# Optimization experiments

Hardware: AMD Instinct MI355X
Metric: run time of the kernel (lower is better)

The kernel has to match this reference:

```python
import jax, jax.numpy as jnp
import numpy as np

B, S, D, H = 2, 2048, 1024, 16  # batch, seq_len, model dim, heads


def setup_inputs() -> dict:
    key = jax.random.key(0)
    ks = jax.random.split(key, 5)
    return {
        "x": jax.random.normal(ks[0], (B, S, D), jnp.float32),
        "idx": jax.random.randint(ks[1], (B,), 0, S),
        "weight": jnp.float32(0.5),
        "attn_forcing": 1,  # static python flag
        "w_qkv": jax.random.normal(ks[2], (D, 3 * D), jnp.float32) * 0.02,
        "b_qkv": jnp.zeros((3 * D,), jnp.float32),
        "w_proj": jax.random.normal(ks[3], (D, D), jnp.float32) * 0.02,
        "b_proj": jnp.zeros((D,), jnp.float32),
    }


def reference(x, idx, weight, attn_forcing, w_qkv, b_qkv, w_proj, b_proj):
    Bx, Sx, Dm = x.shape
    dh = Dm // H
    # qkv projection (Conv1D: x @ w + b)
    qkv = x @ w_qkv + b_qkv  # [B,S,3D]
    q, k, v = jnp.split(qkv, 3, axis=-1)
    q = q.reshape(Bx, Sx, H, dh).transpose(0, 2, 1, 3)  # [B,H,S,dh]
    k = k.reshape(Bx, Sx, H, dh).transpose(0, 2, 1, 3)
    v = v.reshape(Bx, Sx, H, dh).transpose(0, 2, 1, 3)
    alen = jnp.arange(Sx)
    mask = (alen[None, :] <= alen[:, None]).astype(x.dtype)  # [S,S] causal
    w = jnp.einsum('bhqd,bhkd->bhqk', q, k) / jnp.asarray(np.sqrt(dh), x.dtype)
    w = w * mask + jnp.asarray(-1e9, x.dtype) * (1 - mask)
    w = jax.nn.softmax(w, axis=-1)
    if attn_forcing:
        # post-softmax forcing reweight: positions >= idx scaled by weight, then renorm
        a = jnp.where(alen[None, :] >= idx[:, None], weight, jnp.asarray(1.0, x.dtype))  # [B,S]
        w = w * a[:, None, None, :]
        w = w / jnp.sum(w, axis=-1, keepdims=True)
    out = jnp.einsum('bhqk,bhkd->bhqd', w, v)  # [B,H,S,dh]
    out = out.transpose(0, 2, 1, 3).reshape(Bx, Sx, Dm)  # merge heads
    return out @ w_proj + b_proj
```

## Files before the change

kernel.cpp:

```cpp
#include <hip/hip_runtime.h>


typedef __attribute__((ext_vector_type(8))) short short8;
typedef __attribute__((ext_vector_type(4))) float f32x4;

#define MFMA_B16(a, b, c) __builtin_amdgcn_mfma_f32_16x16x32_bf16(a, b, c, 0, 0, 0)

#if __has_builtin(__builtin_amdgcn_exp2f)
#define EXP2(x) __builtin_amdgcn_exp2f(x)
#else
#define EXP2(x) exp2f(x)
#endif

static __device__ __forceinline__ unsigned short f2bf(float f) {
    union { float f; unsigned int u; } v;
    v.f = f;
    unsigned int r = (v.u + 0x7fffu + ((v.u >> 16) & 1u)) >> 16;
    return (unsigned short)r;
}

static __device__ __forceinline__ unsigned int pk_bf16(float a, float b) {
#if __has_builtin(__builtin_amdgcn_cvt_pk_bf16_f32)
    typedef __bf16 bf2 __attribute__((ext_vector_type(2)));
    union { bf2 v; unsigned int u; } c;
    c.v = __builtin_amdgcn_cvt_pk_bf16_f32(a, b);
    return c.u;
#else
    return (unsigned int)f2bf(a) | ((unsigned int)f2bf(b) << 16);
#endif
}

static __device__ __forceinline__ void gl_lds16(const void* g, void* l) {
    __builtin_amdgcn_global_load_lds(
        (const __attribute__((address_space(1))) unsigned int*)g,
        (__attribute__((address_space(3))) unsigned int*)l, 16, 0, 0);
}

__global__ __launch_bounds__(256) void prep_kernel(const float4* __restrict__ x,
                                                   ushort4* __restrict__ xb,
                                                   const float* __restrict__ wqkv,
                                                   unsigned short* __restrict__ wqkvT,
                                                   const float* __restrict__ wproj,
                                                   unsigned short* __restrict__ wprojT) {
    const int bid = blockIdx.x;
    if (bid < 4096) {
        int i = bid * 256 + threadIdx.x;
        float4 v = x[i];
        ushort4 o;
        o.x = f2bf(v.x); o.y = f2bf(v.y); o.z = f2bf(v.z); o.w = f2bf(v.w);
        xb[i] = o;
        return;
    }
    __shared__ float t[32][33];
    const float* in;
    unsigned short* out;
    int R, C, bx, by;
    if (bid < 4096 + 3072) {
        int g = bid - 4096;
        in = wqkv; out = wqkvT; R = 1024; C = 3072;
        bx = g % 96; by = g / 96;
    } else {
        int g = bid - 7168;
        in = wproj; out = wprojT; R = 1024; C = 1024;
        bx = g & 31; by = g >> 5;
    }
    const int c0 = bx * 32, r0 = by * 32;
    const int xx = threadIdx.x & 31, yy0 = threadIdx.x >> 5;
    #pragma unroll
    for (int yy = yy0; yy < 32; yy += 8)
        t[yy][xx] = in[(size_t)(r0 + yy) * C + (c0 + xx)];
    __syncthreads();
    #pragma unroll
    for (int yy = yy0; yy < 32; yy += 8)
        out[(size_t)(c0 + yy) * R + (r0 + xx)] = f2bf(t[xx][yy]);
}

__global__ __launch_bounds__(256) void gemm_qkv_kernel(const unsigned short* __restrict__ A,
                                                       const unsigned short* __restrict__ Bt,
                                                       const float* __restrict__ bias,
                                                       unsigned short* __restrict__ q,
                                                       unsigned short* __restrict__ k,
                                                       unsigned short* __restrict__ vT) {
    __shared__ unsigned short As[128 * 64];
    __shared__ unsigned short Bs[128 * 64];
    const int tid = threadIdx.x;
    const int lane = tid & 63, wave = tid >> 6;
    const int l15 = lane & 15, quad = lane >> 4;
    const int wm = wave >> 1, wn = wave & 1;
    const int row0 = blockIdx.y * 128, col0 = blockIdx.x * 128;
    const int K = 1024;
    const bool isV = (blockIdx.x >= 16);

    int srow[4], scol[4], sdst[4];
    #pragma unroll
    for (int h = 0; h < 4; ++h) {
        int D = h * 256 + wave * 64 + lane;
        srow[h] = D >> 3;
        scol[h] = ((D & 7) ^ (srow[h] & 7)) * 8;
        sdst[h] = (h * 256 + wave * 64) * 8;
    }

    f32x4 acc[4][4] = {};

    for (int kt = 0; kt < K; kt += 64) {
        #pragma unroll
        for (int h = 0; h < 4; ++h) {
            gl_lds16(&A[(size_t)(row0 + srow[h]) * K + kt + scol[h]], &As[sdst[h]]);
            gl_lds16(&Bt[(size_t)(col0 + srow[h]) * K + kt + scol[h]], &Bs[sdst[h]]);
        }
        __syncthreads();
        #pragma unroll
        for (int kk = 0; kk < 2; ++kk) {
            short8 af[4], bf[4];
            #pragma unroll
            for (int i = 0; i < 4; ++i) {
                int r = wm * 64 + i * 16 + l15;
                af[i] = *(const short8*)&As[r * 64 + (((kk * 4 + quad) ^ (r & 7)) * 8)];
            }
            #pragma unroll
            for (int j = 0; j < 4; ++j) {
                int r = wn * 64 + j * 16 + l15;
                bf[j] = *(const short8*)&Bs[r * 64 + (((kk * 4 + quad) ^ (r & 7)) * 8)];
            }
            if (isV) {
                #pragma unroll
                for (int i = 0; i < 4; ++i)
                    #pragma unroll
                    for (int j = 0; j < 4; ++j)
                        acc[i][j] = MFMA_B16(af[i], bf[j], acc[i][j]);
            } else {
                #pragma unroll
                for (int i = 0; i < 4; ++i)
                    #pragma unroll
                    for (int j = 0; j < 4; ++j)
                        acc[i][j] = MFMA_B16(bf[j], af[i], acc[i][j]);
            }
        }
        __syncthreads();
    }

    const int b = row0 >> 11;
    const int s0 = row0 & 2047;
    const float* bb = bias + col0 + wn * 64;

    if (!isV) {
        const int which = blockIdx.x >> 3;
        unsigned short* dst = which ? k : q;
        const float scale = which ? 1.0f : 0.1803368867f;
        const int hh = ((blockIdx.x & 7) << 1) + wn;
        #pragma unroll
        for (int i = 0; i < 4; ++i) {
            const int s = s0 + wm * 64 + i * 16 + l15;
            unsigned short* drow = dst + ((size_t)((b * 16 + hh) * 2048 + s)) * 64;
            #pragma unroll
            for (int j = 0; j < 4; ++j) {
                float4 b4 = ((const float4*)bb)[j * 4 + quad];
                uint2 pv;
                pv.x = pk_bf16((acc[i][j][0] + b4.x) * scale, (acc[i][j][1] + b4.y) * scale);
                pv.y = pk_bf16((acc[i][j][2] + b4.z) * scale, (acc[i][j][3] + b4.w) * scale);
                *(uint2*)&drow[j * 16 + quad * 4] = pv;
            }
        }
    } else {
        const int hh = ((blockIdx.x - 16) << 1) + wn;
        #pragma unroll
        for (int j = 0; j < 4; ++j) {
            const int d = j * 16 + l15;
            const float bv = bb[d];
            unsigned short* drow = vT + ((size_t)((b * 16 + hh) * 64 + d)) * 2048 + s0;
            #pragma unroll
            for (int i = 0; i < 4; ++i) {
                uint2 pv;
                pv.x = pk_bf16(acc[i][j][0] + bv, acc[i][j][1] + bv);
                pv.y = pk_bf16(acc[i][j][2] + bv, acc[i][j][3] + bv);
                *(uint2*)&drow[wm * 64 + i * 16 + quad * 4] = pv;
            }
        }
    }
}

__global__ __launch_bounds__(256) void gemm_proj_kernel(const unsigned short* __restrict__ A,
                                                        const unsigned short* __restrict__ Bt,
                                                        const float* __restrict__ bias,
                                                        float* __restrict__ out) {
    __shared__ unsigned short As[128 * 64];
    __shared__ unsigned short Bs[64 * 64];
    const int tid = threadIdx.x;
    const int lane = tid & 63, wave = tid >> 6;
    const int l15 = lane & 15, quad = lane >> 4;
    const int wm = wave >> 1, wn = wave & 1;
    const int row0 = blockIdx.y * 128, col0 = blockIdx.x * 64;
    const int K = 1024;

    int srow[4], scol[4], sdst[4];
    #pragma unroll
    for (int h = 0; h < 4; ++h) {
        int D = h * 256 + wave * 64 + lane;
        srow[h] = D >> 3;
        scol[h] = ((D & 7) ^ (srow[h] & 7)) * 8;
        sdst[h] = (h * 256 + wave * 64) * 8;
    }

    f32x4 acc[4][2] = {};

    for (int kt = 0; kt < K; kt += 64) {
        #pragma unroll
        for (int h = 0; h < 4; ++h)
            gl_lds16(&A[(size_t)(row0 + srow[h]) * K + kt + scol[h]], &As[sdst[h]]);
        #pragma unroll
        for (int h = 0; h < 2; ++h)
            gl_lds16(&Bt[(size_t)(col0 + srow[h]) * K + kt + scol[h]], &Bs[sdst[h]]);
        __syncthreads();
        #pragma unroll
        for (int kk = 0; kk < 2; ++kk) {
            short8 af[4], bf[2];
            #pragma unroll
            for (int i = 0; i < 4; ++i) {
                int r = wm * 64 + i * 16 + l15;
                af[i] = *(const short8*)&As[r * 64 + (((kk * 4 + quad) ^ (r & 7)) * 8)];
            }
            #pragma unroll
            for (int j = 0; j < 2; ++j) {
                int r = wn * 32 + j * 16 + l15;
                bf[j] = *(const short8*)&Bs[r * 64 + (((kk * 4 + quad) ^ (r & 7)) * 8)];
            }
            #pragma unroll
            for (int i = 0; i < 4; ++i)
                #pragma unroll
                for (int j = 0; j < 2; ++j)
                    acc[i][j] = MFMA_B16(bf[j], af[i], acc[i][j]);
        }
        __syncthreads();
    }

    const float* bb = bias + col0 + wn * 32;
    #pragma unroll
    for (int i = 0; i < 4; ++i) {
        const int row = row0 + wm * 64 + i * 16 + l15;
        #pragma unroll
        for (int j = 0; j < 2; ++j) {
            float4 b4 = ((const float4*)bb)[j * 4 + quad];
            float4 ov;
            ov.x = acc[i][j][0] + b4.x;
            ov.y = acc[i][j][1] + b4.y;
            ov.z = acc[i][j][2] + b4.z;
            ov.w = acc[i][j][3] + b4.w;
            *(float4*)&out[(size_t)row * 1024 + col0 + wn * 32 + j * 16 + quad * 4] = ov;
        }
    }
}

__global__ __launch_bounds__(256) void attn_kernel(const unsigned short* __restrict__ Q,
                                                   const unsigned short* __restrict__ Kg,
                                                   const unsigned short* __restrict__ Vt,
                                                   const int* __restrict__ idx,
                                                   const float* __restrict__ weight,
                                                   const int* __restrict__ forcing,
                                                   unsigned short* __restrict__ O) {
    __shared__ unsigned short Ks[2][4096];
    __shared__ unsigned short Vs[2][4096];
    __shared__ unsigned short Pw[4][1024];

    const int tid = threadIdx.x;
    const int lane = tid & 63, wave = tid >> 6;
    const int l15 = lane & 15, quad = lane >> 4;
    const int bid = blockIdx.x;
    const int u = bid >> 5, a = u & 7, qg = u >> 3;
    const int t = (qg == 0) ? (31 - a) : (qg == 1) ? (16 + a) : (qg == 2) ? (15 - a) : a;
    const int bh = bid & 31;
    const int b = bh >> 4, hh = bh & 15;
    const unsigned short* Qb = Q + (size_t)bh * 2048 * 64;
    const unsigned short* Kh = Kg + (size_t)bh * 2048 * 64;
    const unsigned short* Vh = Vt + (size_t)bh * 2048 * 64;

    const int idxb = idx[b];
    const float lw = (forcing[0] != 0) ? __log2f(weight[0]) : 0.0f;

    const int L0 = wave * 128 + lane;
    const int rS = L0 >> 3;
    const int cS = (L0 & 7) ^ (rS & 7);
    const int ldsOffJ0 = (wave * 128) * 8;
    const int ldsOffJ1 = (wave * 128 + 64) * 8;

    const int q0 = t * 64 + wave * 16;
    const int qrow = q0 + l15;

    short8 aq0 = *(const short8*)&Qb[(q0 + l15) * 64 + quad * 8];
    short8 aq1 = *(const short8*)&Qb[(q0 + l15) * 64 + 32 + quad * 8];

    const short8 ones8 = {0x3F80, 0x3F80, 0x3F80, 0x3F80, 0x3F80, 0x3F80, 0x3F80, 0x3F80};

    f32x4 o[4] = {};
    f32x4 lsum = {};

    const int nkb = t + 1;

    {
        const unsigned short* kg = Kh + (size_t)rS * 64 + cS * 8;
        const unsigned short* vg = Vh + (size_t)rS * 2048 + cS * 8;
        gl_lds16(kg,            &Ks[0][ldsOffJ0]);
        gl_lds16(kg + 8 * 64,   &Ks[0][ldsOffJ1]);
        gl_lds16(vg,            &Vs[0][ldsOffJ0]);
        gl_lds16(vg + 8 * 2048, &Vs[0][ldsOffJ1]);
    }
    __syncthreads();

    unsigned short* const pwb = &Pw[wave][0];
    const int pwr = l15 * 64;
    const int pa7 = l15 & 7;

    for (int kb = 0; kb < nkb; ++kb) {
        const int cur = kb & 1;
        const int kbase = kb * 64;
        if (kb + 1 < nkb) {
            const int nb = kbase + 64;
            const unsigned short* kg = Kh + (size_t)(nb + rS) * 64 + cS * 8;
            const unsigned short* vg = Vh + (size_t)rS * 2048 + nb + cS * 8;
            gl_lds16(kg,            &Ks[cur ^ 1][ldsOffJ0]);
            gl_lds16(kg + 8 * 64,   &Ks[cur ^ 1][ldsOffJ1]);
            gl_lds16(vg,            &Vs[cur ^ 1][ldsOffJ0]);
            gl_lds16(vg + 8 * 2048, &Vs[cur ^ 1][ldsOffJ1]);
        }

        const bool fullF = (kbase >= idxb);
        const bool bndF = (!fullF) && (kbase + 63 >= idxb);
        const float zu = fullF ? lw : 0.0f;

        f32x4 sT[4];
        #pragma unroll
        for (int kt = 0; kt < 4; ++kt) {
            const int row = kt * 16 + l15;
            short8 k0 = *(const short8*)&Ks[cur][row * 64 + ((quad ^ (row & 7)) * 8)];
            short8 k1 = *(const short8*)&Ks[cur][row * 64 + (((4 + quad) ^ (row & 7)) * 8)];
            f32x4 z;
            if (!bndF) {
                z[0] = zu; z[1] = zu; z[2] = zu; z[3] = zu;
            } else {
                #pragma unroll
                for (int r = 0; r < 4; ++r)
                    z[r] = (kbase + kt * 16 + quad * 4 + r >= idxb) ? lw : 0.0f;
            }
            z = MFMA_B16(k0, aq0, z);
            z = MFMA_B16(k1, aq1, z);
            sT[kt] = z;
        }

        if (kb == t) {
            #pragma unroll
            for (int kt = 0; kt < 4; ++kt)
                #pragma unroll
                for (int r = 0; r < 4; ++r)
                    if (kbase + kt * 16 + quad * 4 + r > qrow) sT[kt][r] = -3.0e38f;
        }

        #pragma unroll
        for (int kt = 0; kt < 4; ++kt)
            #pragma unroll
            for (int r = 0; r < 4; ++r)
                sT[kt][r] = EXP2(sT[kt][r]);

        #pragma unroll
        for (int kt = 0; kt < 4; ++kt) {
            unsigned int* pw = (unsigned int*)&pwb[pwr +
                (((kt * 2 + (quad >> 1)) ^ pa7) * 8) + (quad & 1) * 4];
            pw[0] = pk_bf16(sT[kt][0], sT[kt][1]);
            pw[1] = pk_bf16(sT[kt][2], sT[kt][3]);
        }

        short8 bp0 = *(const short8*)&pwb[pwr + ((quad ^ pa7) * 8)];
        short8 bp1 = *(const short8*)&pwb[pwr + (((4 + quad) ^ pa7) * 8)];

        lsum = MFMA_B16(ones8, bp0, lsum);
        lsum = MFMA_B16(ones8, bp1, lsum);

        #pragma unroll
        for (int dt = 0; dt < 4; ++dt) {
            const int row = dt * 16 + l15;
            short8 vf0 = *(const short8*)&Vs[cur][row * 64 + ((quad ^ (row & 7)) * 8)];
            short8 vf1 = *(const short8*)&Vs[cur][row * 64 + (((4 + quad) ^ (row & 7)) * 8)];
            f32x4 oo = o[dt];
            oo = MFMA_B16(vf0, bp0, oo);
            oo = MFMA_B16(vf1, bp1, oo);
            o[dt] = oo;
        }

        __syncthreads();
    }

    const float inv = 1.0f / lsum[0];
    unsigned short* sc = &Ks[0][0] + wave * 1152;
    #pragma unroll
    for (int dt = 0; dt < 4; ++dt)
        #pragma unroll
        for (int r = 0; r < 4; ++r)
            sc[l15 * 72 + dt * 16 + quad * 4 + r] = f2bf(o[dt][r] * inv);
    const size_t rowoff = ((size_t)(b * 2048 + q0 + l15)) * 1024 + hh * 64;
    #pragma unroll
    for (int h = 0; h < 2; ++h) {
        short8 v8 = *(const short8*)&sc[l15 * 72 + quad * 16 + h * 8];
        *(short8*)&O[rowoff + quad * 16 + h * 8] = v8;
    }
}

extern "C" void kernel_launch(void* const* d_in, const int* in_sizes, int n_in,
                              void* d_out, int out_size, void* d_ws, size_t ws_size,
                              hipStream_t stream) {
    const float* x        = (const float*)d_in[0];
    const int*   idx      = (const int*)d_in[1];
    const float* weight   = (const float*)d_in[2];
    const int*   forcing  = (const int*)d_in[3];
    const float* w_qkv    = (const float*)d_in[4];
    const float* b_qkv    = (const float*)d_in[5];
    const float* w_proj   = (const float*)d_in[6];
    const float* b_proj   = (const float*)d_in[7];
    float* out = (float*)d_out;

    char* ws = (char*)d_ws;
    unsigned short* xb      = (unsigned short*)(ws);
    unsigned short* wqkvT   = (unsigned short*)(ws + 8388608);
    unsigned short* wprojT  = (unsigned short*)(ws + 14680064);
    unsigned short* qbuf    = (unsigned short*)(ws + 16777216);
    unsigned short* kbuf    = (unsigned short*)(ws + 25165824);
    unsigned short* vTbuf   = (unsigned short*)(ws + 33554432);
    unsigned short* attn_out = xb;

    prep_kernel<<<8192, 256, 0, stream>>>((const float4*)x, (ushort4*)xb,
                                          w_qkv, wqkvT, w_proj, wprojT);
    gemm_qkv_kernel<<<dim3(24, 32), 256, 0, stream>>>(xb, wqkvT, b_qkv, qbuf, kbuf, vTbuf);
    attn_kernel<<<1024, 256, 0, stream>>>(qbuf, kbuf, vTbuf, idx, weight, forcing, attn_out);
    gemm_proj_kernel<<<dim3(16, 32), 256, 0, stream>>>(attn_out, wprojT, b_proj, out);
}
```

Measured before the change: 186.4 us.

## Deepen K/V prefetch to two tiles with explicit vmcnt waits and barriers

Restructures the attention loop so K/V tiles are prefetched two iterations ahead. Explicit s_waitcnt vmcnt and raw s_barrier replace __syncthreads, so only the current tile's loads are waited on. Block-to-(head, query tile) mapping changes to launch the heaviest causal tiles first, spread across heads. MFMA groups are wrapped in s_setprio to favour matrix work among waves. This risks races if the vmcnt counts do not match the issued loads, e.g. when other global loads are outstanding.

```diff
diff --git a/kernel.cpp b/kernel.cpp
--- a/kernel.cpp
+++ b/kernel.cpp
@@ -265,9 +265,9 @@
     const int lane = tid & 63, wave = tid >> 6;
     const int l15 = lane & 15, quad = lane >> 4;
     const int bid = blockIdx.x;
-    const int u = bid >> 5, a = u & 7, qg = u >> 3;
-    const int t = (qg == 0) ? (31 - a) : (qg == 1) ? (16 + a) : (qg == 2) ? (15 - a) : a;
-    const int bh = bid & 31;
+    const int u = bid >> 3;
+    const int bh = ((bid & 7) << 2) + (u & 3);
+    const int t = 31 - (u >> 2);
     const int b = bh >> 4, hh = bh & 15;
     const unsigned short* Qb = Q + (size_t)bh * 2048 * 64;
     const unsigned short* Kh = Kg + (size_t)bh * 2048 * 64;
@@ -302,8 +302,13 @@
         gl_lds16(kg + 8 * 64,   &Ks[0][ldsOffJ1]);
         gl_lds16(vg,            &Vs[0][ldsOffJ0]);
         gl_lds16(vg + 8 * 2048, &Vs[0][ldsOffJ1]);
-    }
-    __syncthreads();
+        if (nkb > 1) {
+            gl_lds16(kg + 64 * 64,          &Ks[1][ldsOffJ0]);
+            gl_lds16(kg + 64 * 64 + 8 * 64, &Ks[1][ldsOffJ1]);
+            gl_lds16(vg + 64,               &Vs[1][ldsOffJ0]);
+            gl_lds16(vg + 64 + 8 * 2048,    &Vs[1][ldsOffJ1]);
+        }
+    }
 
     unsigned short* const pwb = &Pw[wave][0];
     const int pwr = l15 * 64;
@@ -312,15 +317,15 @@
     for (int kb = 0; kb < nkb; ++kb) {
         const int cur = kb & 1;
         const int kbase = kb * 64;
+
         if (kb + 1 < nkb) {
-            const int nb = kbase + 64;
-            const unsigned short* kg = Kh + (size_t)(nb + rS) * 64 + cS * 8;
-            const unsigned short* vg = Vh + (size_t)rS * 2048 + nb + cS * 8;
-            gl_lds16(kg,            &Ks[cur ^ 1][ldsOffJ0]);
-            gl_lds16(kg + 8 * 64,   &Ks[cur ^ 1][ldsOffJ1]);
-            gl_lds16(vg,            &Vs[cur ^ 1][ldsOffJ0]);
-            gl_lds16(vg + 8 * 2048, &Vs[cur ^ 1][ldsOffJ1]);
-        }
+            asm volatile("s_waitcnt vmcnt(4)" ::: "memory");
+        } else {
+            asm volatile("s_waitcnt vmcnt(0)" ::: "memory");
+        }
+        __builtin_amdgcn_sched_barrier(0);
+        __builtin_amdgcn_s_barrier();
+        __builtin_amdgcn_sched_barrier(0);
 
         const bool fullF = (kbase >= idxb);
         const bool bndF = (!fullF) && (kbase + 63 >= idxb);
@@ -340,8 +345,10 @@
                 for (int r = 0; r < 4; ++r)
                     z[r] = (kbase + kt * 16 + quad * 4 + r >= idxb) ? lw : 0.0f;
             }
+            __builtin_amdgcn_s_setprio(1);
             z = MFMA_B16(k0, aq0, z);
             z = MFMA_B16(k1, aq1, z);
+            __builtin_amdgcn_s_setprio(0);
             sT[kt] = z;
         }
 
@@ -370,8 +377,10 @@
         short8 bp0 = *(const short8*)&pwb[pwr + ((quad ^ pa7) * 8)];
         short8 bp1 = *(const short8*)&pwb[pwr + (((4 + quad) ^ pa7) * 8)];
 
+        __builtin_amdgcn_s_setprio(1);
         lsum = MFMA_B16(ones8, bp0, lsum);
         lsum = MFMA_B16(ones8, bp1, lsum);
+        __builtin_amdgcn_s_setprio(0);
 
         #pragma unroll
         for (int dt = 0; dt < 4; ++dt) {
@@ -379,12 +388,27 @@
             short8 vf0 = *(const short8*)&Vs[cur][row * 64 + ((quad ^ (row & 7)) * 8)];
             short8 vf1 = *(const short8*)&Vs[cur][row * 64 + (((4 + quad) ^ (row & 7)) * 8)];
             f32x4 oo = o[dt];
+            __builtin_amdgcn_s_setprio(1);
             oo = MFMA_B16(vf0, bp0, oo);
             oo = MFMA_B16(vf1, bp1, oo);
+            __builtin_amdgcn_s_setprio(0);
             o[dt] = oo;
         }
 
-        __syncthreads();
+        asm volatile("s_waitcnt lgkmcnt(0)" ::: "memory");
+        __builtin_amdgcn_sched_barrier(0);
+        __builtin_amdgcn_s_barrier();
+        __builtin_amdgcn_sched_barrier(0);
+
+        if (kb + 2 < nkb) {
+            const int nb = kbase + 128;
+            const unsigned short* kg = Kh + (size_t)(nb + rS) * 64 + cS * 8;
+            const unsigned short* vg = Vh + (size_t)rS * 2048 + nb + cS * 8;
+            gl_lds16(kg,            &Ks[cur][ldsOffJ0]);
+            gl_lds16(kg + 8 * 64,   &Ks[cur][ldsOffJ1]);
+            gl_lds16(vg,            &Vs[cur][ldsOffJ0]);
+            gl_lds16(vg + 8 * 2048, &Vs[cur][ldsOffJ1]);
+        }
     }
 
     const float inv = 1.0f / lsum[0];
```

Measured after the change: 189.1 us. No clear change (+1.5%).

## Pair complementary causal query tiles in one 512-thread attention block sharing K/V tiles

Applied to the files above, without the earlier changes.

Each attention block now holds two query tiles, t and 31-t, for the same head, using 8 waves instead of 4. K/V tiles streamed into LDS are shared by both halves, and the waves for the short tile go idle once their causal range ends. This balances work across blocks and halves the K/V global-to-LDS traffic for the shorter tile. In exchange, the short-tile waves still sit through every barrier, and the larger block may lower occupancy.

```diff
diff --git a/kernel.cpp b/kernel.cpp
--- a/kernel.cpp
+++ b/kernel.cpp
@@ -250,24 +250,23 @@
     }
 }
 
-__global__ __launch_bounds__(256) void attn_kernel(const unsigned short* __restrict__ Q,
+__global__ __launch_bounds__(512) void attn_kernel(const unsigned short* __restrict__ Q,
                                                    const unsigned short* __restrict__ Kg,
                                                    const unsigned short* __restrict__ Vt,
                                                    const int* __restrict__ idx,
                                                    const float* __restrict__ weight,
                                                    const int* __restrict__ forcing,
                                                    unsigned short* __restrict__ O) {
-    __shared__ unsigned short Ks[2][4096];
-    __shared__ unsigned short Vs[2][4096];
-    __shared__ unsigned short Pw[4][1024];
+    __shared__ unsigned short smem[24576];
 
     const int tid = threadIdx.x;
     const int lane = tid & 63, wave = tid >> 6;
     const int l15 = lane & 15, quad = lane >> 4;
     const int bid = blockIdx.x;
-    const int u = bid >> 5, a = u & 7, qg = u >> 3;
-    const int t = (qg == 0) ? (31 - a) : (qg == 1) ? (16 + a) : (qg == 2) ? (15 - a) : a;
-    const int bh = bid & 31;
+    const int g = bid >> 3;
+    const int bh = ((bid & 7) << 2) + (g & 3);
+    const int p = g >> 2;
+    const int tA = 31 - p, tB = p;
     const int b = bh >> 4, hh = bh & 15;
     const unsigned short* Qb = Q + (size_t)bh * 2048 * 64;
     const unsigned short* Kh = Kg + (size_t)bh * 2048 * 64;
@@ -276,14 +275,15 @@
     const int idxb = idx[b];
     const float lw = (forcing[0] != 0) ? __log2f(weight[0]) : 0.0f;
 
-    const int L0 = wave * 128 + lane;
-    const int rS = L0 >> 3;
-    const int cS = (L0 & 7) ^ (rS & 7);
-    const int ldsOffJ0 = (wave * 128) * 8;
-    const int ldsOffJ1 = (wave * 128 + 64) * 8;
-
-    const int q0 = t * 64 + wave * 16;
+    const int wq = (wave < 4) ? tA : tB;
+    const int wg = wave & 3;
+    const int q0 = wq * 64 + wg * 16;
     const int qrow = q0 + l15;
+    const int nkb = tA + 1;
+    const int nkbw = wq + 1;
+
+    const int rS = tid >> 3;
+    const int cS8 = ((tid & 7) ^ (rS & 7)) * 8;
 
     short8 aq0 = *(const short8*)&Qb[(q0 + l15) * 64 + quad * 8];
     short8 aq1 = *(const short8*)&Qb[(q0 + l15) * 64 + 32 + quad * 8];
@@ -293,19 +293,11 @@
     f32x4 o[4] = {};
     f32x4 lsum = {};
 
-    const int nkb = t + 1;
-
-    {
-        const unsigned short* kg = Kh + (size_t)rS * 64 + cS * 8;
-        const unsigned short* vg = Vh + (size_t)rS * 2048 + cS * 8;
-        gl_lds16(kg,            &Ks[0][ldsOffJ0]);
-        gl_lds16(kg + 8 * 64,   &Ks[0][ldsOffJ1]);
-        gl_lds16(vg,            &Vs[0][ldsOffJ0]);
-        gl_lds16(vg + 8 * 2048, &Vs[0][ldsOffJ1]);
-    }
+    gl_lds16(Kh + (size_t)rS * 64 + cS8,   &smem[tid * 8]);
+    gl_lds16(Vh + (size_t)rS * 2048 + cS8, &smem[8192 + tid * 8]);
     __syncthreads();
 
-    unsigned short* const pwb = &Pw[wave][0];
+    unsigned short* const pwb = &smem[16384 + wave * 1024];
     const int pwr = l15 * 64;
     const int pa7 = l15 & 7;
 
@@ -314,81 +306,82 @@
         const int kbase = kb * 64;
         if (kb + 1 < nkb) {
             const int nb = kbase + 64;
-            const unsigned short* kg = Kh + (size_t)(nb + rS) * 64 + cS * 8;
-            const unsigned short* vg = Vh + (size_t)rS * 2048 + nb + cS * 8;
-            gl_lds16(kg,            &Ks[cur ^ 1][ldsOffJ0]);
-            gl_lds16(kg + 8 * 64,   &Ks[cur ^ 1][ldsOffJ1]);
-            gl_lds16(vg,            &Vs[cur ^ 1][ldsOffJ0]);
-            gl_lds16(vg + 8 * 2048, &Vs[cur ^ 1][ldsOffJ1]);
-        }
-
-        const bool fullF = (kbase >= idxb);
-        const bool bndF = (!fullF) && (kbase + 63 >= idxb);
-        const float zu = fullF ? lw : 0.0f;
-
-        f32x4 sT[4];
-        #pragma unroll
-        for (int kt = 0; kt < 4; ++kt) {
-            const int row = kt * 16 + l15;
-            short8 k0 = *(const short8*)&Ks[cur][row * 64 + ((quad ^ (row & 7)) * 8)];
-            short8 k1 = *(const short8*)&Ks[cur][row * 64 + (((4 + quad) ^ (row & 7)) * 8)];
-            f32x4 z;
-            if (!bndF) {
-                z[0] = zu; z[1] = zu; z[2] = zu; z[3] = zu;
-            } else {
+            gl_lds16(Kh + (size_t)(nb + rS) * 64 + cS8,      &smem[(cur ^ 1) * 4096 + tid * 8]);
+            gl_lds16(Vh + (size_t)rS * 2048 + nb + cS8,      &smem[8192 + (cur ^ 1) * 4096 + tid * 8]);
+        }
+
+        if (kb < nkbw) {
+            const unsigned short* KsP = &smem[cur * 4096];
+            const unsigned short* VsP = &smem[8192 + cur * 4096];
+
+            const bool fullF = (kbase >= idxb);
+            const bool bndF = (!fullF) && (kbase + 63 >= idxb);
+            const float zu = fullF ? lw : 0.0f;
+
+            f32x4 sT[4];
+            #pragma unroll
+            for (int kt = 0; kt < 4; ++kt) {
+                const int row = kt * 16 + l15;
+                short8 k0 = *(const short8*)&KsP[row * 64 + ((quad ^ (row & 7)) * 8)];
+                short8 k1 = *(const short8*)&KsP[row * 64 + (((4 + quad) ^ (row & 7)) * 8)];
+                f32x4 z;
+                if (!bndF) {
+                    z[0] = zu; z[1] = zu; z[2] = zu; z[3] = zu;
+                } else {
+                    #pragma unroll
+                    for (int r = 0; r < 4; ++r)
+                        z[r] = (kbase + kt * 16 + quad * 4 + r >= idxb) ? lw : 0.0f;
+                }
+                z = MFMA_B16(k0, aq0, z);
+                z = MFMA_B16(k1, aq1, z);
+                sT[kt] = z;
+            }
+
+            if (kb == wq) {
                 #pragma unroll
-                for (int r = 0; r < 4; ++r)
-                    z[r] = (kbase + kt * 16 + quad * 4 + r >= idxb) ? lw : 0.0f;
-            }
-            z = MFMA_B16(k0, aq0, z);
-            z = MFMA_B16(k1, aq1, z);
-            sT[kt] = z;
-        }
-
-        if (kb == t) {
+                for (int kt = 0; kt < 4; ++kt)
+                    #pragma unroll
+                    for (int r = 0; r < 4; ++r)
+                        if (kbase + kt * 16 + quad * 4 + r > qrow) sT[kt][r] = -3.0e38f;
+            }
+
             #pragma unroll
             for (int kt = 0; kt < 4; ++kt)
                 #pragma unroll
                 for (int r = 0; r < 4; ++r)
-                    if (kbase + kt * 16 + quad * 4 + r > qrow) sT[kt][r] = -3.0e38f;
-        }
-
-        #pragma unroll
-        for (int kt = 0; kt < 4; ++kt)
-            #pragma unroll
-            for (int r = 0; r < 4; ++r)
-                sT[kt][r] = EXP2(sT[kt][r]);
-
-        #pragma unroll
-        for (int kt = 0; kt < 4; ++kt) {
-            unsigned int* pw = (unsigned int*)&pwb[pwr +
-                (((kt * 2 + (quad >> 1)) ^ pa7) * 8) + (quad & 1) * 4];
-            pw[0] = pk_bf16(sT[kt][0], sT[kt][1]);
-            pw[1] = pk_bf16(sT[kt][2], sT[kt][3]);
-        }
-
-        short8 bp0 = *(const short8*)&pwb[pwr + ((quad ^ pa7) * 8)];
-        short8 bp1 = *(const short8*)&pwb[pwr + (((4 + quad) ^ pa7) * 8)];
-
-        lsum = MFMA_B16(ones8, bp0, lsum);
-        lsum = MFMA_B16(ones8, bp1, lsum);
-
-        #pragma unroll
-        for (int dt = 0; dt < 4; ++dt) {
-            const int row = dt * 16 + l15;
-            short8 vf0 = *(const short8*)&Vs[cur][row * 64 + ((quad ^ (row & 7)) * 8)];
-            short8 vf1 = *(const short8*)&Vs[cur][row * 64 + (((4 + quad) ^ (row & 7)) * 8)];
-            f32x4 oo = o[dt];
-            oo = MFMA_B16(vf0, bp0, oo);
-            oo = MFMA_B16(vf1, bp1, oo);
-            o[dt] = oo;
+                    sT[kt][r] = EXP2(sT[kt][r]);
+
+            #pragma unroll
+            for (int kt = 0; kt < 4; ++kt) {
+                unsigned int* pw = (unsigned int*)&pwb[pwr +
+                    (((kt * 2 + (quad >> 1)) ^ pa7) * 8) + (quad & 1) * 4];
+                pw[0] = pk_bf16(sT[kt][0], sT[kt][1]);
+                pw[1] = pk_bf16(sT[kt][2], sT[kt][3]);
+            }
+
+            short8 bp0 = *(const short8*)&pwb[pwr + ((quad ^ pa7) * 8)];
+            short8 bp1 = *(const short8*)&pwb[pwr + (((4 + quad) ^ pa7) * 8)];
+
+            lsum = MFMA_B16(ones8, bp0, lsum);
+            lsum = MFMA_B16(ones8, bp1, lsum);
+
+            #pragma unroll
+            for (int dt = 0; dt < 4; ++dt) {
+                const int row = dt * 16 + l15;
+                short8 vf0 = *(const short8*)&VsP[row * 64 + ((quad ^ (row & 7)) * 8)];
+                short8 vf1 = *(const short8*)&VsP[row * 64 + (((4 + quad) ^ (row & 7)) * 8)];
+                f32x4 oo = o[dt];
+                oo = MFMA_B16(vf0, bp0, oo);
+                oo = MFMA_B16(vf1, bp1, oo);
+                o[dt] = oo;
+            }
         }
 
         __syncthreads();
     }
 
     const float inv = 1.0f / lsum[0];
-    unsigned short* sc = &Ks[0][0] + wave * 1152;
+    unsigned short* sc = &smem[wave * 1152];
     #pragma unroll
     for (int dt = 0; dt < 4; ++dt)
         #pragma unroll
@@ -427,6 +420,6 @@
     prep_kernel<<<8192, 256, 0, stream>>>((const float4*)x, (ushort4*)xb,
                                           w_qkv, wqkvT, w_proj, wprojT);
     gemm_qkv_kernel<<<dim3(24, 32), 256, 0, stream>>>(xb, wqkvT, b_qkv, qbuf, kbuf, vTbuf);
-    attn_kernel<<<1024, 256, 0, stream>>>(qbuf, kbuf, vTbuf, idx, weight, forcing, attn_out);
+    attn_kernel<<<512, 512, 0, stream>>>(qbuf, kbuf, vTbuf, idx, weight, forcing, attn_out);
     gemm_proj_kernel<<<dim3(16, 32), 256, 0, stream>>>(attn_out, wprojT, b_proj, out);
 }
```

New measurement: 188.3 us. No clear change (+1.0%).
